# Optimization experiments

Hardware: AMD Instinct MI355X
Metric: run time of the kernel (lower is better)

Reference implementation:

```python
import jax, jax.numpy as jnp
import numpy as np

SP_BETA = 1.0       # rendering_options.sp_beta
INF_DELTA = 1e10    # use_inf_depth=True -> last delta is 1e10
EPS = 1e-10


def setup_inputs() -> dict:
    key = jax.random.key(0)
    k1, k2, k3 = jax.random.split(key, 3)
    B, R, S, C = 8, 16384, 64, 3  # batch, rays, samples-per-ray, rgb channels
    colors = jax.random.normal(k1, (B, R, S, C), dtype=jnp.float32)
    densities = jax.random.normal(k2, (B, R, S, 1), dtype=jnp.float32)
    # depths must be sorted (increasing) along the sample dimension
    depths = jnp.sort(
        jax.random.uniform(k3, (B, R, S, 1), dtype=jnp.float32, minval=0.1, maxval=6.0),
        axis=2,
    )
    return {"colors": colors, "densities": densities, "depths": depths}


def reference(colors, densities, depths):
    # deltas between consecutive samples, last delta = 1e10 (infinite far plane)
    deltas = depths[:, :, 1:] - depths[:, :, :-1]                      # [B,R,S-1,1]
    deltas = jnp.concatenate(
        [deltas, jnp.full_like(deltas[:, :, :1], INF_DELTA)], axis=2)  # [B,R,S,1]

    # clamp_mode == 'softplus' with beta=1.0: softplus(x*beta)/beta
    dens = jax.nn.softplus(densities * SP_BETA) / SP_BETA              # [B,R,S,1]

    alphas = 1.0 - jnp.exp(-deltas * dens)                             # [B,R,S,1]

    # transmittance: cumulative product of (1-alpha), with leading ones
    trans = jnp.cumprod(1.0 - alphas + EPS, axis=2)                    # [B,R,S,1]
    trans = jnp.concatenate([jnp.ones_like(trans[:, :, :1]), trans], axis=2)  # [B,R,S+1,1]

    final_transmittance = trans[:, :, -1, 0]                           # [B,R]
    weights = alphas * trans[:, :, :-1]                                # [B,R,S,1]

    rgb_final = (weights * colors).sum(axis=2)                         # [B,R,C]
    depth = (weights * depths).sum(axis=2)                             # [B,R,1]
    return rgb_final, depth, weights, final_transmittance
```

## Files before the change

kernel.cpp:

```cpp
#include <hip/hip_runtime.h>

#define INF_DELTA 1e10f
#define RM_EPS 1e-10f
#define LOG2E 1.4426950408889634f

typedef float floatx4 __attribute__((ext_vector_type(4)));

__device__ __forceinline__ int   f2i(float x){ union{float f;int i;}u; u.f=x; return u.i; }
__device__ __forceinline__ float i2f(int x)  { union{int i;float f;}u; u.i=x; return u.f; }

template<int CTRL>
__device__ __forceinline__ float dpp_mov(float src, float old){
    return i2f(__builtin_amdgcn_update_dpp(f2i(old), f2i(src), CTRL, 0xF, 0xF, false));
}

__device__ __forceinline__ float softplus_log2(float x) {
    const float q  = __builtin_amdgcn_exp2f(-__builtin_fabsf(x) * LOG2E);
    const float l2 = __builtin_amdgcn_logf(1.0f + q);
    return __builtin_fmaf(__builtin_fmaxf(x, 0.0f), LOG2E, l2);
}

__global__ __launch_bounds__(256) void raymarch_kernel(
    const float4* __restrict__ colors4,
    const float4* __restrict__ densities4,
    const float4* __restrict__ depths4,
    float* __restrict__ rgb_out,
    float* __restrict__ depth_out,
    float4* __restrict__ weights4,
    float* __restrict__ trans_out,
    int n_rays)
{
    const int tid = threadIdx.x;
    const int sl  = tid & 15;
    const int ray = blockIdx.x * 16 + (tid >> 4);
    if (ray >= n_rays) return;

    const long vbase = (long)ray * 16 + sl;

    const float4 d4 = depths4[vbase];
    const float4 x4 = densities4[vbase];
    const float4* cp = colors4 + (long)ray * 48 + sl * 3;
    const float4 ca = cp[0], cb = cp[1], cc = cp[2];

    const float dnext = dpp_mov<0x101>(d4.x, 0.0f);
    const float del0 = d4.y - d4.x;
    const float del1 = d4.z - d4.y;
    const float del2 = d4.w - d4.z;
    const float del3 = (sl == 15) ? INF_DELTA : (dnext - d4.w);

    const float y0 = __builtin_amdgcn_exp2f(-del0 * softplus_log2(x4.x));
    const float y1 = __builtin_amdgcn_exp2f(-del1 * softplus_log2(x4.y));
    const float y2 = __builtin_amdgcn_exp2f(-del2 * softplus_log2(x4.z));
    const float y3 = __builtin_amdgcn_exp2f(-del3 * softplus_log2(x4.w));

    const float t0 = y0 + RM_EPS, t1 = y1 + RM_EPS;
    const float t2 = y2 + RM_EPS, t3 = y3 + RM_EPS;

    const float ex1 = t0, ex2 = t0 * t1, ex3 = ex2 * t2;
    const float ptot = ex3 * t3;

    const float e0 = (1.0f - y0);
    const float e1 = (1.0f - y1) * ex1;
    const float e2 = (1.0f - y2) * ex2;
    const float e3 = (1.0f - y3) * ex3;

    float s0 = e0*ca.x + e1*ca.w + e2*cb.z + e3*cc.y;
    float s1 = e0*ca.y + e1*cb.x + e2*cb.w + e3*cc.z;
    float s2 = e0*ca.z + e1*cb.y + e2*cc.x + e3*cc.w;
    float s3 = e0*d4.x + e1*d4.y + e2*d4.z + e3*d4.w;

    float P = ptot;
    P *= dpp_mov<0x111>(P, 1.0f);
    P *= dpp_mov<0x112>(P, 1.0f);
    P *= dpp_mov<0x114>(P, 1.0f);
    P *= dpp_mov<0x118>(P, 1.0f);
    const float Pexcl = dpp_mov<0x111>(P, 1.0f);

    floatx4 wv;
    wv.x = e0 * Pexcl; wv.y = e1 * Pexcl; wv.z = e2 * Pexcl; wv.w = e3 * Pexcl;
    __builtin_nontemporal_store(wv, (floatx4*)&weights4[vbase]);

    float v0 = Pexcl * s0, v1 = Pexcl * s1, v2 = Pexcl * s2, v3 = Pexcl * s3;
    v0 += dpp_mov<0x111>(v0, 0.0f); v0 += dpp_mov<0x112>(v0, 0.0f);
    v0 += dpp_mov<0x114>(v0, 0.0f); v0 += dpp_mov<0x118>(v0, 0.0f);
    v1 += dpp_mov<0x111>(v1, 0.0f); v1 += dpp_mov<0x112>(v1, 0.0f);
    v1 += dpp_mov<0x114>(v1, 0.0f); v1 += dpp_mov<0x118>(v1, 0.0f);
    v2 += dpp_mov<0x111>(v2, 0.0f); v2 += dpp_mov<0x112>(v2, 0.0f);
    v2 += dpp_mov<0x114>(v2, 0.0f); v2 += dpp_mov<0x118>(v2, 0.0f);
    v3 += dpp_mov<0x111>(v3, 0.0f); v3 += dpp_mov<0x112>(v3, 0.0f);
    v3 += dpp_mov<0x114>(v3, 0.0f); v3 += dpp_mov<0x118>(v3, 0.0f);

    if (sl == 15) {
        const long r3 = (long)ray * 3;
        rgb_out[r3 + 0] = v0;
        rgb_out[r3 + 1] = v1;
        rgb_out[r3 + 2] = v2;
        depth_out[ray]  = v3;
        trans_out[ray]  = P;
    }
}

extern "C" void kernel_launch(void* const* d_in, const int* in_sizes, int n_in,
                              void* d_out, int out_size, void* d_ws, size_t ws_size,
                              hipStream_t stream) {
    const float4* colors4    = (const float4*)d_in[0];
    const float4* densities4 = (const float4*)d_in[1];
    const float4* depths4    = (const float4*)d_in[2];

    const int n_rays = in_sizes[1] / 64;

    float* out      = (float*)d_out;
    float* rgb      = out;
    float* depth_o  = rgb + (long)n_rays * 3;
    float4* weights = (float4*)(depth_o + n_rays);
    float* trans    = (float*)(weights + (long)n_rays * 16);

    const int blocks = (n_rays + 15) / 16;
    raymarch_kernel<<<blocks, 256, 0, stream>>>(
        colors4, densities4, depths4, rgb, depth_o, weights, trans, n_rays);
}
```

Measured before the change: 202.5 us.

## Coalesce color loads via LDS transpose and software-prefetch multiple rays per wave

Each wave now handles 16 rays in four iterations of four rays. Colors are loaded with fully coalesced lane-contiguous float4 reads and reshuffled through shared memory into per-lane sample order. The next iteration's inputs are prefetched into registers while the current one computes. This targets the strided color loads and the limited memory-level parallelism of one-ray-per-16-lanes. In exchange the grid is four times smaller, register pressure rises, and LDS round trips are added within the wave.

```diff
diff --git a/kernel.cpp b/kernel.cpp
--- a/kernel.cpp
+++ b/kernel.cpp
@@ -6,15 +6,15 @@
 
 typedef float floatx4 __attribute__((ext_vector_type(4)));
 
-__device__ __forceinline__ int   f2i(float x){ union{float f;int i;}u; u.f=x; return u.i; }
-__device__ __forceinline__ float i2f(int x)  { union{int i;float f;}u; u.i=x; return u.f; }
+static __device__ __forceinline__ int   f2i(float x){ union{float f;int i;}u; u.f=x; return u.i; }
+static __device__ __forceinline__ float i2f(int x)  { union{int i;float f;}u; u.i=x; return u.f; }
 
 template<int CTRL>
-__device__ __forceinline__ float dpp_mov(float src, float old){
+static __device__ __forceinline__ float dpp_mov(float src, float old){
     return i2f(__builtin_amdgcn_update_dpp(f2i(old), f2i(src), CTRL, 0xF, 0xF, false));
 }
 
-__device__ __forceinline__ float softplus_log2(float x) {
+static __device__ __forceinline__ float softplus_log2(float x) {
     const float q  = __builtin_amdgcn_exp2f(-__builtin_fabsf(x) * LOG2E);
     const float l2 = __builtin_amdgcn_logf(1.0f + q);
     return __builtin_fmaf(__builtin_fmaxf(x, 0.0f), LOG2E, l2);
@@ -30,73 +30,112 @@
     float* __restrict__ trans_out,
     int n_rays)
 {
-    const int tid = threadIdx.x;
-    const int sl  = tid & 15;
-    const int ray = blockIdx.x * 16 + (tid >> 4);
-    if (ray >= n_rays) return;
+    __shared__ float4 lds_c[4][192];
 
-    const long vbase = (long)ray * 16 + sl;
+    const int tid  = threadIdx.x;
+    const int lane = tid & 63;
+    const int wave = tid >> 6;
+    const int sl   = lane & 15;
+    const int rsub = lane >> 4;
 
-    const float4 d4 = depths4[vbase];
-    const float4 x4 = densities4[vbase];
-    const float4* cp = colors4 + (long)ray * 48 + sl * 3;
-    const float4 ca = cp[0], cb = cp[1], cc = cp[2];
+    const int wave_ray_base = blockIdx.x * 64 + wave * 16;
 
-    const float dnext = dpp_mov<0x101>(d4.x, 0.0f);
-    const float del0 = d4.y - d4.x;
-    const float del1 = d4.z - d4.y;
-    const float del2 = d4.w - d4.z;
-    const float del3 = (sl == 15) ? INF_DELTA : (dnext - d4.w);
+    float4 nd4 = {}, nx4 = {}, nc0 = {}, nc1 = {}, nc2 = {};
+    if (wave_ray_base < n_rays) {
+        const long cb = (long)wave_ray_base * 48;
+        nc0 = colors4[cb + lane];
+        nc1 = colors4[cb + 64 + lane];
+        nc2 = colors4[cb + 128 + lane];
+        const long vb = (long)wave_ray_base * 16 + lane;
+        nd4 = depths4[vb];
+        nx4 = densities4[vb];
+    }
 
-    const float y0 = __builtin_amdgcn_exp2f(-del0 * softplus_log2(x4.x));
-    const float y1 = __builtin_amdgcn_exp2f(-del1 * softplus_log2(x4.y));
-    const float y2 = __builtin_amdgcn_exp2f(-del2 * softplus_log2(x4.z));
-    const float y3 = __builtin_amdgcn_exp2f(-del3 * softplus_log2(x4.w));
+    #pragma unroll
+    for (int i = 0; i < 4; ++i) {
+        const int rb = wave_ray_base + i * 4;
+        if (rb >= n_rays) break;
 
-    const float t0 = y0 + RM_EPS, t1 = y1 + RM_EPS;
-    const float t2 = y2 + RM_EPS, t3 = y3 + RM_EPS;
+        const float4 d4 = nd4, x4 = nx4;
+        const float4 c0 = nc0, c1 = nc1, c2 = nc2;
 
-    const float ex1 = t0, ex2 = t0 * t1, ex3 = ex2 * t2;
-    const float ptot = ex3 * t3;
+        const int rb2 = rb + 4;
+        if (i + 1 < 4 && rb2 < n_rays) {
+            const long cb = (long)rb2 * 48;
+            nc0 = colors4[cb + lane];
+            nc1 = colors4[cb + 64 + lane];
+            nc2 = colors4[cb + 128 + lane];
+            const long vb = (long)rb2 * 16 + lane;
+            nd4 = depths4[vb];
+            nx4 = densities4[vb];
+        }
 
-    const float e0 = (1.0f - y0);
-    const float e1 = (1.0f - y1) * ex1;
-    const float e2 = (1.0f - y2) * ex2;
-    const float e3 = (1.0f - y3) * ex3;
+        lds_c[wave][lane]       = c0;
+        lds_c[wave][64 + lane]  = c1;
+        lds_c[wave][128 + lane] = c2;
+        const int ci = rsub * 48 + sl * 3;
+        const float4 ca  = lds_c[wave][ci];
+        const float4 cbv = lds_c[wave][ci + 1];
+        const float4 cc  = lds_c[wave][ci + 2];
 
-    float s0 = e0*ca.x + e1*ca.w + e2*cb.z + e3*cc.y;
-    float s1 = e0*ca.y + e1*cb.x + e2*cb.w + e3*cc.z;
-    float s2 = e0*ca.z + e1*cb.y + e2*cc.x + e3*cc.w;
-    float s3 = e0*d4.x + e1*d4.y + e2*d4.z + e3*d4.w;
+        const float dnext = dpp_mov<0x101>(d4.x, 0.0f);
+        const float del0 = d4.y - d4.x;
+        const float del1 = d4.z - d4.y;
+        const float del2 = d4.w - d4.z;
+        const float del3 = (sl == 15) ? INF_DELTA : (dnext - d4.w);
 
-    float P = ptot;
-    P *= dpp_mov<0x111>(P, 1.0f);
-    P *= dpp_mov<0x112>(P, 1.0f);
-    P *= dpp_mov<0x114>(P, 1.0f);
-    P *= dpp_mov<0x118>(P, 1.0f);
-    const float Pexcl = dpp_mov<0x111>(P, 1.0f);
+        const float y0 = __builtin_amdgcn_exp2f(-del0 * softplus_log2(x4.x));
+        const float y1 = __builtin_amdgcn_exp2f(-del1 * softplus_log2(x4.y));
+        const float y2 = __builtin_amdgcn_exp2f(-del2 * softplus_log2(x4.z));
+        const float y3 = __builtin_amdgcn_exp2f(-del3 * softplus_log2(x4.w));
 
-    floatx4 wv;
-    wv.x = e0 * Pexcl; wv.y = e1 * Pexcl; wv.z = e2 * Pexcl; wv.w = e3 * Pexcl;
-    __builtin_nontemporal_store(wv, (floatx4*)&weights4[vbase]);
+        const float t0 = y0 + RM_EPS, t1 = y1 + RM_EPS;
+        const float t2 = y2 + RM_EPS, t3 = y3 + RM_EPS;
 
-    float v0 = Pexcl * s0, v1 = Pexcl * s1, v2 = Pexcl * s2, v3 = Pexcl * s3;
-    v0 += dpp_mov<0x111>(v0, 0.0f); v0 += dpp_mov<0x112>(v0, 0.0f);
-    v0 += dpp_mov<0x114>(v0, 0.0f); v0 += dpp_mov<0x118>(v0, 0.0f);
-    v1 += dpp_mov<0x111>(v1, 0.0f); v1 += dpp_mov<0x112>(v1, 0.0f);
-    v1 += dpp_mov<0x114>(v1, 0.0f); v1 += dpp_mov<0x118>(v1, 0.0f);
-    v2 += dpp_mov<0x111>(v2, 0.0f); v2 += dpp_mov<0x112>(v2, 0.0f);
-    v2 += dpp_mov<0x114>(v2, 0.0f); v2 += dpp_mov<0x118>(v2, 0.0f);
-    v3 += dpp_mov<0x111>(v3, 0.0f); v3 += dpp_mov<0x112>(v3, 0.0f);
-    v3 += dpp_mov<0x114>(v3, 0.0f); v3 += dpp_mov<0x118>(v3, 0.0f);
+        const float ex1 = t0, ex2 = t0 * t1, ex3 = ex2 * t2;
+        const float ptot = ex3 * t3;
 
-    if (sl == 15) {
-        const long r3 = (long)ray * 3;
-        rgb_out[r3 + 0] = v0;
-        rgb_out[r3 + 1] = v1;
-        rgb_out[r3 + 2] = v2;
-        depth_out[ray]  = v3;
-        trans_out[ray]  = P;
+        const float e0 = (1.0f - y0);
+        const float e1 = (1.0f - y1) * ex1;
+        const float e2 = (1.0f - y2) * ex2;
+        const float e3 = (1.0f - y3) * ex3;
+
+        const float s0 = e0*ca.x + e1*ca.w  + e2*cbv.z + e3*cc.y;
+        const float s1 = e0*ca.y + e1*cbv.x + e2*cbv.w + e3*cc.z;
+        const float s2 = e0*ca.z + e1*cbv.y + e2*cc.x  + e3*cc.w;
+        const float s3 = e0*d4.x + e1*d4.y  + e2*d4.z  + e3*d4.w;
+
+        float P = ptot;
+        P *= dpp_mov<0x111>(P, 1.0f);
+        P *= dpp_mov<0x112>(P, 1.0f);
+        P *= dpp_mov<0x114>(P, 1.0f);
+        P *= dpp_mov<0x118>(P, 1.0f);
+        const float Pexcl = dpp_mov<0x111>(P, 1.0f);
+
+        const long vbase = (long)(rb + rsub) * 16 + sl;
+        floatx4 wv;
+        wv.x = e0 * Pexcl; wv.y = e1 * Pexcl; wv.z = e2 * Pexcl; wv.w = e3 * Pexcl;
+        __builtin_nontemporal_store(wv, (floatx4*)&weights4[vbase]);
+
+        float v0 = Pexcl * s0, v1 = Pexcl * s1, v2 = Pexcl * s2, v3 = Pexcl * s3;
+        v0 += dpp_mov<0x111>(v0, 0.0f); v0 += dpp_mov<0x112>(v0, 0.0f);
+        v0 += dpp_mov<0x114>(v0, 0.0f); v0 += dpp_mov<0x118>(v0, 0.0f);
+        v1 += dpp_mov<0x111>(v1, 0.0f); v1 += dpp_mov<0x112>(v1, 0.0f);
+        v1 += dpp_mov<0x114>(v1, 0.0f); v1 += dpp_mov<0x118>(v1, 0.0f);
+        v2 += dpp_mov<0x111>(v2, 0.0f); v2 += dpp_mov<0x112>(v2, 0.0f);
+        v2 += dpp_mov<0x114>(v2, 0.0f); v2 += dpp_mov<0x118>(v2, 0.0f);
+        v3 += dpp_mov<0x111>(v3, 0.0f); v3 += dpp_mov<0x112>(v3, 0.0f);
+        v3 += dpp_mov<0x114>(v3, 0.0f); v3 += dpp_mov<0x118>(v3, 0.0f);
+
+        if (sl == 15) {
+            const int ray = rb + rsub;
+            const long r3 = (long)ray * 3;
+            rgb_out[r3 + 0] = v0;
+            rgb_out[r3 + 1] = v1;
+            rgb_out[r3 + 2] = v2;
+            depth_out[ray]  = v3;
+            trans_out[ray]  = P;
+        }
     }
 }
 
@@ -115,7 +154,7 @@
     float4* weights = (float4*)(depth_o + n_rays);
     float* trans    = (float*)(weights + (long)n_rays * 16);
 
-    const int blocks = (n_rays + 15) / 16;
+    const int blocks = (n_rays + 63) / 64;
     raymarch_kernel<<<blocks, 256, 0, stream>>>(
         colors4, densities4, depths4, rgb, depth_o, weights, trans, n_rays);
 }
```

Measured after the change: 207.1 us. 1.02x slower.
